# Performance work log

Hardware: AMD Instinct MI355X
Metric: run time of the kernel (lower is better)

Reference implementation:

```python
import jax, jax.numpy as jnp
import numpy as np

B, L, H, HD, FD = 1, 1024, 32, 64, 64
HID = H * HD
EPS = 1e-12


def setup_inputs() -> dict:
    key = jax.random.key(0)
    ks = jax.random.split(key, 7)
    s = 1.0 / np.sqrt(HID)
    return {
        "hidden_states": jax.random.normal(ks[0], (B, L, HID), dtype=jnp.float32),
        "Wq": jax.random.normal(ks[1], (HID, HID), dtype=jnp.float32) * s,
        "Wk": jax.random.normal(ks[2], (HID, HID), dtype=jnp.float32) * s,
        "Wv": jax.random.normal(ks[3], (HID, HID), dtype=jnp.float32) * s,
        "Wo": jax.random.normal(ks[4], (HID, HID), dtype=jnp.float32) * s,
        "Wfq": jax.random.normal(ks[5], (H, HD, FD), dtype=jnp.float32) * (1.0 / np.sqrt(HD)),
        "Wfk": jax.random.normal(ks[6], (H, HD, FD), dtype=jnp.float32) * (1.0 / np.sqrt(HD)),
    }


def _heads(x):
    # [b, l, hid] -> [b, h, l, hd]
    b, l, _ = x.shape
    return x.reshape(b, l, H, HD).transpose(0, 2, 1, 3)


def _feature_map(x, Wf):
    # per-head learned kernel + softmax over feature dim (hedgehog-style)
    z = jnp.einsum('bhld,hdf->bhlf', x, Wf)
    return jax.nn.softmax(z, axis=-1)


def _linear_attention(q, k, v, eps=EPS):
    # causal_dot_product: cumsum of outer-product KV state (fp32)
    qf, kf, vf = q.astype(jnp.float32), k.astype(jnp.float32), v.astype(jnp.float32)
    kv = jnp.cumsum(jnp.einsum('bhlf,bhld->bhlfd', kf, vf), axis=2)  # [b,h,l,f,d]
    y = jnp.einsum('bhlf,bhlfd->bhld', qf, kv)
    # fp32_attention=False branch: normalizer computed on cumsum(k)
    k_cum = jnp.cumsum(kf, axis=2).astype(q.dtype)
    denom = jnp.einsum('bhld,bhld->bhl', q, k_cum) + eps
    return y.astype(q.dtype) / denom[..., None]


def reference(hidden_states, Wq, Wk, Wv, Wo, Wfq, Wfk):
    b, l, _ = hidden_states.shape
    q = _heads(hidden_states @ Wq.T)
    k = _heads(hidden_states @ Wk.T)
    v = _heads(hidden_states @ Wv.T)
    fq = _feature_map(q, Wfq)
    fk = _feature_map(k, Wfk)
    y = _linear_attention(fq, fk, v)  # [b,h,l,hd]
    y = y.transpose(0, 2, 1, 3).reshape(b, l, HID)
    return y @ Wo.T
```

## Files before the change

kernel.cpp:

```cpp
#include <hip/hip_runtime.h>
#include <math.h>

constexpr int LQ  = 1024;
constexpr int NH  = 32;
constexpr int HDM = 64;
constexpr int FDM = 64;
constexpr int HID = 2048;
constexpr int NCH = 16;
constexpr int CT  = 64;
#define EPSV 1e-12f

typedef __bf16 bf16x8 __attribute__((ext_vector_type(8)));
typedef float  f32x4  __attribute__((ext_vector_type(4)));

__device__ __forceinline__ unsigned short f2b_raw(float x) {
    union { float f; unsigned int u; } v; v.f = x;
    unsigned int r = v.u + 0x7fffu + ((v.u >> 16) & 1u);
    return (unsigned short)(r >> 16);
}
__device__ __forceinline__ float b2f(ushort u) {
    union { unsigned int i; float f; } v; v.i = ((unsigned int)u) << 16; return v.f;
}

#define ASYNC16(ldsp, gp) __builtin_amdgcn_global_load_lds( \
    (const __attribute__((address_space(1))) void*)(gp),    \
    (__attribute__((address_space(3))) void*)(ldsp), 16, 0, 0)

template <bool BF16OUT>
__device__ __forceinline__ void gemm_body(const ushort* __restrict__ A,
                                          const ushort* __restrict__ B,
                                          void* __restrict__ Cv,
                                          int M, int N, int K) {
    __shared__ __align__(16) ushort As[64 * 32];
    __shared__ __align__(16) ushort Bs[128 * 32];
    const int t    = threadIdx.x;
    const int wave = t >> 6, lane = t & 63;
    const int wr   = (wave >> 1) * 32;
    const int wc   = (wave & 1) * 64;
    const int bm   = blockIdx.y * 64, bn = blockIdx.x * 128;

    const int lrow = lane >> 2;
    const int lk   = (lane & 3) * 8;
    const ushort* ga  = A + (size_t)(bm + wave * 16 + lrow) * K + lk;
    const ushort* gb0 = B + (size_t)(bn + wave * 32 + lrow) * K + lk;
    const ushort* gb1 = gb0 + 16 * (size_t)K;
    ushort* la  = As + (wave * 16) * 32;
    ushort* lb0 = Bs + (wave * 32) * 32;
    ushort* lb1 = lb0 + 16 * 32;

    const int fr = lane & 15;
    const int fo = (lane >> 4) * 8;

    f32x4 acc[2][4] = {};

    for (int k0 = 0; k0 < K; k0 += 32) {
        __syncthreads();
        ASYNC16(la, ga); ASYNC16(lb0, gb0); ASYNC16(lb1, gb1);
        ga += 32; gb0 += 32; gb1 += 32;
        __syncthreads();
        bf16x8 af[2], bg[4];
#pragma unroll
        for (int i = 0; i < 2; ++i) af[i] = *(const bf16x8*)&As[(wr + i * 16 + fr) * 32 + fo];
#pragma unroll
        for (int j = 0; j < 4; ++j) bg[j] = *(const bf16x8*)&Bs[(wc + j * 16 + fr) * 32 + fo];
#pragma unroll
        for (int i = 0; i < 2; ++i)
#pragma unroll
            for (int j = 0; j < 4; ++j)
                acc[i][j] = __builtin_amdgcn_mfma_f32_16x16x32_bf16(af[i], bg[j], acc[i][j], 0, 0, 0);
    }

    const int er = (lane >> 4) * 4;
    const int ec = lane & 15;
#pragma unroll
    for (int i = 0; i < 2; ++i)
#pragma unroll
        for (int j = 0; j < 4; ++j) {
            const size_t base = (size_t)(bm + wr + i * 16 + er) * N + bn + wc + j * 16 + ec;
            if constexpr (BF16OUT) {
                ushort* C = (ushort*)Cv;
#pragma unroll
                for (int r = 0; r < 4; ++r) C[base + (size_t)r * N] = f2b_raw(acc[i][j][r]);
            } else {
                float* C = (float*)Cv;
#pragma unroll
                for (int r = 0; r < 4; ++r) C[base + (size_t)r * N] = acc[i][j][r];
            }
        }
}

__global__ __launch_bounds__(256) void gemm_qkv(const ushort* __restrict__ hsb,
                                                const ushort* __restrict__ wqb,
                                                const ushort* __restrict__ wkb,
                                                const ushort* __restrict__ wvb,
                                                ushort* __restrict__ qb,
                                                ushort* __restrict__ kb,
                                                ushort* __restrict__ vb) {
    const ushort* B; ushort* C;
    if (blockIdx.z == 0)      { B = wqb; C = qb; }
    else if (blockIdx.z == 1) { B = wkb; C = kb; }
    else                      { B = wvb; C = vb; }
    gemm_body<true>(hsb, B, C, LQ, HID, HID);
}

__global__ __launch_bounds__(256) void gemm_one(const ushort* __restrict__ A,
                                                const ushort* __restrict__ B,
                                                float* __restrict__ C) {
    gemm_body<false>(A, B, C, LQ, HID, HID);
}

struct F2BArgs { const float* src[5]; ushort* dst[5]; int n[5]; };
__global__ __launch_bounds__(256) void f2b_multi(F2BArgs p) {
    const int which = blockIdx.y;
    const float* s = p.src[which];
    ushort* d = p.dst[which];
    const int n = p.n[which];
    const int i = (blockIdx.x * 256 + threadIdx.x) * 4;
    if (i >= n) return;
    float4 v = *(const float4*)&s[i];
    ushort4 o = make_ushort4(f2b_raw(v.x), f2b_raw(v.y), f2b_raw(v.z), f2b_raw(v.w));
    *(ushort4*)&d[i] = o;
}

__global__ __launch_bounds__(256) void wf_transpose(const float* __restrict__ Wfq,
                                                    const float* __restrict__ Wfk,
                                                    ushort* __restrict__ WfqT,
                                                    ushort* __restrict__ WfkT) {
    const int h = blockIdx.x, isK = blockIdx.y;
    const float* src = (isK ? Wfk : Wfq) + (size_t)h * 4096;
    ushort* dst = (isK ? WfkT : WfqT) + (size_t)h * 4096;
    __shared__ float tile[64][65];
    const int t = threadIdx.x;
    for (int it = 0; it < 16; ++it) {
        int e = it * 256 + t; int d = e >> 6, f = e & 63;
        tile[d][f] = src[e];
    }
    __syncthreads();
    for (int it = 0; it < 16; ++it) {
        int e = it * 256 + t; int f = e >> 6, d = e & 63;
        dst[e] = f2b_raw(tile[d][f]);
    }
}

__global__ __launch_bounds__(256) void featmap_chunk(
    const ushort* __restrict__ qb, const ushort* __restrict__ kb,
    const ushort* __restrict__ vb,
    const ushort* __restrict__ WfqT, const ushort* __restrict__ WfkT,
    ushort* __restrict__ fqB, ushort* __restrict__ fkB,
    ushort* __restrict__ VTb, float* __restrict__ Sraw, float* __restrict__ Ks) {
    __shared__ __align__(16) ushort Xs[64 * 72];
    __shared__ __align__(16) ushort Ws[64 * 72];
    __shared__ float Zs[64][68];
    __shared__ __align__(16) ushort Fs[64 * 72];
    __shared__ __align__(16) ushort Vs[64 * 72];

    const int c = blockIdx.x, h = blockIdx.y, isK = blockIdx.z;
    const int t = threadIdx.x, lane = t & 63, wave = t >> 6;
    const int l0 = c * CT;
    const int fr = lane & 15, fo = (lane >> 4) * 8;
    const int g = lane >> 4, cc = lane & 15;

    const ushort* X  = (isK ? kb : qb);
    const ushort* WT = (isK ? WfkT : WfqT) + (size_t)h * 4096;

    for (int it = 0; it < 2; ++it) {
        int e = (it * 256 + t) * 8;
        int row = e >> 6, col = e & 63;
        *(uint4*)&Xs[row * 72 + col] = *(const uint4*)&X[(size_t)(l0 + row) * HID + h * HDM + col];
        *(uint4*)&Ws[row * 72 + col] = *(const uint4*)&WT[e];
        if (isK) {
            uint4 vv = *(const uint4*)&vb[(size_t)(l0 + row) * HID + h * HDM + col];
            const ushort* pv = (const ushort*)&vv;
#pragma unroll
            for (int i = 0; i < 8; ++i) Vs[(col + i) * 72 + row] = pv[i];
        }
    }
    __syncthreads();

    f32x4 accZ[4] = {};
#pragma unroll
    for (int kp = 0; kp < 2; ++kp) {
        bf16x8 a = *(const bf16x8*)&Xs[(wave * 16 + fr) * 72 + kp * 32 + fo];
#pragma unroll
        for (int j = 0; j < 4; ++j) {
            bf16x8 b = *(const bf16x8*)&Ws[(j * 16 + fr) * 72 + kp * 32 + fo];
            accZ[j] = __builtin_amdgcn_mfma_f32_16x16x32_bf16(a, b, accZ[j], 0, 0, 0);
        }
    }
#pragma unroll
    for (int j = 0; j < 4; ++j)
#pragma unroll
        for (int r = 0; r < 4; ++r)
            Zs[wave * 16 + g * 4 + r][j * 16 + cc] = accZ[j][r];
    __syncthreads();

    const int srow = t >> 2, spart = t & 3;
    float zv[16], m = -1e30f;
#pragma unroll
    for (int i = 0; i < 16; ++i) { zv[i] = Zs[srow][spart * 16 + i]; m = fmaxf(m, zv[i]); }
    m = fmaxf(m, __shfl_xor(m, 1)); m = fmaxf(m, __shfl_xor(m, 2));
    float s = 0.f;
#pragma unroll
    for (int i = 0; i < 16; ++i) { zv[i] = __expf(zv[i] - m); s += zv[i]; }
    s += __shfl_xor(s, 1); s += __shfl_xor(s, 2);
    const float inv = 1.0f / s;
    ushort ov[16];
#pragma unroll
    for (int i = 0; i < 16; ++i) ov[i] = f2b_raw(zv[i] * inv);
    ushort* outp = (isK ? fkB : fqB) + ((size_t)h * LQ + l0 + srow) * FDM + spart * 16;
    *(uint4*)&outp[0] = *(uint4*)&ov[0];
    *(uint4*)&outp[8] = *(uint4*)&ov[8];
    if (isK) {
#pragma unroll
        for (int i = 0; i < 16; ++i) Fs[(spart * 16 + i) * 72 + srow] = ov[i];
    }
    if (!isK) return;
    __syncthreads();

    if (t < 64) {
        float ks = 0.f;
#pragma unroll 8
        for (int l = 0; l < 64; ++l) ks += b2f(Fs[t * 72 + l]);
        Ks[((size_t)h * NCH + c) * FDM + t] = ks;
    }
    const size_t cb = ((size_t)h * NCH + c) * 4096;
    for (int it = 0; it < 2; ++it) {
        int e = (it * 256 + t) * 8;
        int row = e >> 6, col = e & 63;
        *(uint4*)&VTb[cb + e] = *(const uint4*)&Vs[row * 72 + col];
    }
    f32x4 accS[4] = {};
#pragma unroll
    for (int kp = 0; kp < 2; ++kp) {
        bf16x8 a = *(const bf16x8*)&Vs[(wave * 16 + fr) * 72 + kp * 32 + fo];
#pragma unroll
        for (int j = 0; j < 4; ++j) {
            bf16x8 b = *(const bf16x8*)&Fs[(j * 16 + fr) * 72 + kp * 32 + fo];
            accS[j] = __builtin_amdgcn_mfma_f32_16x16x32_bf16(a, b, accS[j], 0, 0, 0);
        }
    }
    float* sp = Sraw + cb;
#pragma unroll
    for (int j = 0; j < 4; ++j)
#pragma unroll
        for (int r = 0; r < 4; ++r)
            sp[(wave * 16 + g * 4 + r) * 64 + j * 16 + cc] = accS[j][r];
}

__global__ __launch_bounds__(256) void prefix2(const float* __restrict__ Sraw,
                                               ushort* __restrict__ SpreB,
                                               const float* __restrict__ Ks,
                                               float* __restrict__ Kpre) {
    const int h = blockIdx.x, eb = blockIdx.y, t = threadIdx.x;
    const int e0 = eb * 512 + t * 2;
    float r0 = 0.f, r1 = 0.f;
    const size_t hb = (size_t)h * NCH * 4096;
    for (int c2 = 0; c2 < NCH; ++c2) {
        const size_t base = hb + (size_t)c2 * 4096 + e0;
        float c0 = Sraw[base], c1 = Sraw[base + 1];
        ushort2 o = make_ushort2(f2b_raw(r0), f2b_raw(r1));
        *(ushort2*)&SpreB[base] = o;
        r0 += c0; r1 += c1;
    }
    if (eb == 0 && t < 64) {
        float rk = 0.f;
        for (int c2 = 0; c2 < NCH; ++c2) {
            const size_t kb2 = ((size_t)h * NCH + c2) * FDM + t;
            float cur = Ks[kb2];
            Kpre[kb2] = rk;
            rk += cur;
        }
    }
}

__global__ __launch_bounds__(256) void intra2(
    const ushort* __restrict__ fqB, const ushort* __restrict__ fkB,
    const ushort* __restrict__ VTb, const ushort* __restrict__ SpreB,
    const float* __restrict__ Kpre, ushort* __restrict__ Yb) {
    __shared__ __align__(16) ushort fqs[64 * 72];
    __shared__ __align__(16) ushort fks[64 * 72];
    __shared__ __align__(16) ushort VTs[64 * 72];
    __shared__ __align__(16) ushort Sps[64 * 72];
    __shared__ __align__(16) ushort Pms[64 * 72];
    __shared__ float den[64], kpr[64];

    const int c = blockIdx.x, h = blockIdx.y;
    const int t = threadIdx.x, lane = t & 63, wave = t >> 6;
    const int l0 = c * CT;
    const int fr = lane & 15, fo = (lane >> 4) * 8;
    const int g = lane >> 4, cc = lane & 15;

    const size_t qkbase = ((size_t)h * LQ + l0) * FDM;
    const size_t cbase  = ((size_t)h * NCH + c) * 4096;
    for (int it = 0; it < 2; ++it) {
        int e = (it * 256 + t) * 8;
        int row = e >> 6, col = e & 63;
        *(uint4*)&fqs[row * 72 + col] = *(const uint4*)&fqB[qkbase + e];
        *(uint4*)&fks[row * 72 + col] = *(const uint4*)&fkB[qkbase + e];
        *(uint4*)&VTs[row * 72 + col] = *(const uint4*)&VTb[cbase + e];
        *(uint4*)&Sps[row * 72 + col] = *(const uint4*)&SpreB[cbase + e];
    }
    if (t < 64) kpr[t] = Kpre[((size_t)h * NCH + c) * FDM + t];
    __syncthreads();

    f32x4 accP[4] = {};
#pragma unroll
    for (int kp = 0; kp < 2; ++kp) {
        bf16x8 a = *(const bf16x8*)&fqs[(wave * 16 + fr) * 72 + kp * 32 + fo];
#pragma unroll
        for (int j = 0; j < 4; ++j) {
            bf16x8 b = *(const bf16x8*)&fks[(j * 16 + fr) * 72 + kp * 32 + fo];
            accP[j] = __builtin_amdgcn_mfma_f32_16x16x32_bf16(a, b, accP[j], 0, 0, 0);
        }
    }
#pragma unroll
    for (int j = 0; j < 4; ++j)
#pragma unroll
        for (int r = 0; r < 4; ++r) {
            int l = wave * 16 + g * 4 + r, lp = j * 16 + cc;
            Pms[l * 72 + lp] = (lp <= l) ? f2b_raw(accP[j][r]) : (ushort)0;
        }
    __syncthreads();

    {
        const int srow = t >> 2, spart = t & 3;
        float s = 0.f;
#pragma unroll
        for (int i = 0; i < 16; ++i) s += b2f(Pms[srow * 72 + spart * 16 + i]);
#pragma unroll
        for (int i = 0; i < 16; ++i) s += b2f(fqs[srow * 72 + spart * 16 + i]) * kpr[spart * 16 + i];
        s += __shfl_xor(s, 1); s += __shfl_xor(s, 2);
        if (spart == 0) den[srow] = s + EPSV;
    }
    __syncthreads();

    f32x4 accY[4] = {};
#pragma unroll
    for (int kp = 0; kp < 2; ++kp) {
        bf16x8 a = *(const bf16x8*)&Pms[(wave * 16 + fr) * 72 + kp * 32 + fo];
#pragma unroll
        for (int j = 0; j < 4; ++j) {
            bf16x8 b = *(const bf16x8*)&VTs[(j * 16 + fr) * 72 + kp * 32 + fo];
            accY[j] = __builtin_amdgcn_mfma_f32_16x16x32_bf16(a, b, accY[j], 0, 0, 0);
        }
    }
#pragma unroll
    for (int kp = 0; kp < 2; ++kp) {
        bf16x8 a = *(const bf16x8*)&fqs[(wave * 16 + fr) * 72 + kp * 32 + fo];
#pragma unroll
        for (int j = 0; j < 4; ++j) {
            bf16x8 b = *(const bf16x8*)&Sps[(j * 16 + fr) * 72 + kp * 32 + fo];
            accY[j] = __builtin_amdgcn_mfma_f32_16x16x32_bf16(a, b, accY[j], 0, 0, 0);
        }
    }
#pragma unroll
    for (int r = 0; r < 4; ++r) {
        int l = wave * 16 + g * 4 + r;
        float inv = 1.0f / den[l];
        ushort* yo = Yb + (size_t)(l0 + l) * HID + h * HDM;
#pragma unroll
        for (int j = 0; j < 4; ++j)
            yo[j * 16 + cc] = f2b_raw(accY[j][r] * inv);
    }
}

extern "C" void kernel_launch(void* const* d_in, const int* in_sizes, int n_in,
                              void* d_out, int out_size, void* d_ws, size_t ws_size,
                              hipStream_t stream) {
    const float* hs  = (const float*)d_in[0];
    const float* Wq  = (const float*)d_in[1];
    const float* Wk  = (const float*)d_in[2];
    const float* Wv  = (const float*)d_in[3];
    const float* Wo  = (const float*)d_in[4];
    const float* Wfq = (const float*)d_in[5];
    const float* Wfk = (const float*)d_in[6];
    float* out = (float*)d_out;

    const size_t SZ = (size_t)LQ * HID;
    const size_t WZ = (size_t)HID * HID;

    char* w = (char*)d_ws;
    auto aus = [&](size_t n) { ushort* p = (ushort*)w; w += n * sizeof(ushort); return p; };
    auto afl = [&](size_t n) { float*  p = (float*)w;  w += n * sizeof(float);  return p; };

    ushort* hsb   = aus(SZ);
    ushort* wqb   = aus(WZ);
    ushort* wkb   = aus(WZ);
    ushort* wvb   = aus(WZ);
    ushort* wob   = aus(WZ);
    ushort* qb2   = aus(SZ);
    ushort* kb2   = aus(SZ);
    ushort* vb2   = aus(SZ);
    ushort* fqB   = aus(SZ);
    ushort* fkB   = aus(SZ);
    ushort* VTb   = aus(SZ);
    ushort* WfqT  = aus((size_t)NH * 4096);
    ushort* WfkT  = aus((size_t)NH * 4096);
    ushort* SpreB = aus(SZ);
    ushort* Yb    = aus(SZ);
    float*  Sraw  = afl(SZ);
    float*  Ks    = afl((size_t)NH * NCH * FDM);
    float*  Kpre  = afl((size_t)NH * NCH * FDM);

    F2BArgs fa;
    fa.src[0] = hs; fa.dst[0] = hsb; fa.n[0] = (int)SZ;
    fa.src[1] = Wq; fa.dst[1] = wqb; fa.n[1] = (int)WZ;
    fa.src[2] = Wk; fa.dst[2] = wkb; fa.n[2] = (int)WZ;
    fa.src[3] = Wv; fa.dst[3] = wvb; fa.n[3] = (int)WZ;
    fa.src[4] = Wo; fa.dst[4] = wob; fa.n[4] = (int)WZ;
    f2b_multi<<<dim3((unsigned)(WZ / 1024), 5), 256, 0, stream>>>(fa);

    wf_transpose<<<dim3(NH, 2), 256, 0, stream>>>(Wfq, Wfk, WfqT, WfkT);

    gemm_qkv<<<dim3(HID / 128, LQ / 64, 3), 256, 0, stream>>>(hsb, wqb, wkb, wvb, qb2, kb2, vb2);

    featmap_chunk<<<dim3(NCH, NH, 2), 256, 0, stream>>>(qb2, kb2, vb2, WfqT, WfkT,
                                                        fqB, fkB, VTb, Sraw, Ks);

    prefix2<<<dim3(NH, 8), 256, 0, stream>>>(Sraw, SpreB, Ks, Kpre);

    intra2<<<dim3(NCH, NH), 256, 0, stream>>>(fqB, fkB, VTb, SpreB, Kpre, Yb);

    gemm_one<<<dim3(HID / 128, LQ / 64), 256, 0, stream>>>(Yb, wob, out);
}
```

Baseline: 212.8 us.

## Double-buffer GEMM LDS tiles with K=64 steps and XOR swizzle

Replaces the GEMM body with a templated core that uses double-buffered LDS tiles and steps K by 64 instead of 32. The next tile's async global-to-LDS loads are issued before computing on the current tile, which roughly halves the barriers per K step. An XOR swizzle on the LDS layout is meant to avoid bank conflicts. The output GEMM switches to 64x64 tiles to launch more blocks, at the cost of doubled shared memory and lower per-block reuse.

```diff
diff --git a/kernel.cpp b/kernel.cpp
--- a/kernel.cpp
+++ b/kernel.cpp
@@ -26,56 +26,85 @@
     (const __attribute__((address_space(1))) void*)(gp),    \
     (__attribute__((address_space(3))) void*)(ldsp), 16, 0, 0)
 
-template <bool BF16OUT>
-__device__ __forceinline__ void gemm_body(const ushort* __restrict__ A,
+template <int TM, int TN, bool BF16OUT>
+__device__ __forceinline__ void gemm_core(const ushort* __restrict__ A,
                                           const ushort* __restrict__ B,
                                           void* __restrict__ Cv,
                                           int M, int N, int K) {
-    __shared__ __align__(16) ushort As[64 * 32];
-    __shared__ __align__(16) ushort Bs[128 * 32];
-    const int t    = threadIdx.x;
-    const int wave = t >> 6, lane = t & 63;
-    const int wr   = (wave >> 1) * 32;
-    const int wc   = (wave & 1) * 64;
-    const int bm   = blockIdx.y * 64, bn = blockIdx.x * 128;
-
-    const int lrow = lane >> 2;
-    const int lk   = (lane & 3) * 8;
-    const ushort* ga  = A + (size_t)(bm + wave * 16 + lrow) * K + lk;
-    const ushort* gb0 = B + (size_t)(bn + wave * 32 + lrow) * K + lk;
-    const ushort* gb1 = gb0 + 16 * (size_t)K;
-    ushort* la  = As + (wave * 16) * 32;
-    ushort* lb0 = Bs + (wave * 32) * 32;
-    ushort* lb1 = lb0 + 16 * 32;
-
-    const int fr = lane & 15;
-    const int fo = (lane >> 4) * 8;
-
-    f32x4 acc[2][4] = {};
-
-    for (int k0 = 0; k0 < K; k0 += 32) {
-        __syncthreads();
-        ASYNC16(la, ga); ASYNC16(lb0, gb0); ASYNC16(lb1, gb1);
-        ga += 32; gb0 += 32; gb1 += 32;
-        __syncthreads();
-        bf16x8 af[2], bg[4];
-#pragma unroll
-        for (int i = 0; i < 2; ++i) af[i] = *(const bf16x8*)&As[(wr + i * 16 + fr) * 32 + fo];
-#pragma unroll
-        for (int j = 0; j < 4; ++j) bg[j] = *(const bf16x8*)&Bs[(wc + j * 16 + fr) * 32 + fo];
-#pragma unroll
-        for (int i = 0; i < 2; ++i)
-#pragma unroll
-            for (int j = 0; j < 4; ++j)
-                acc[i][j] = __builtin_amdgcn_mfma_f32_16x16x32_bf16(af[i], bg[j], acc[i][j], 0, 0, 0);
-    }
-
-    const int er = (lane >> 4) * 4;
+    constexpr int FI = TM / 32, FJ = TN / 32;
+    constexpr int AI = TM / 32, BJ = TN / 32;
+    constexpr int ASZ = TM * 64, BSZ = TN * 64;
+    __shared__ __align__(16) ushort As[2 * ASZ];
+    __shared__ __align__(16) ushort Bs[2 * BSZ];
+
+    const int t = threadIdx.x, wave = t >> 6, lane = t & 63;
+    const int wr = (wave >> 1) * (TM / 2), wc = (wave & 1) * (TN / 2);
+    const int bm = blockIdx.y * TM, bn = blockIdx.x * TN;
+
+    const int grow = lane >> 3;
+    const int gsw  = ((lane & 7) ^ (grow & 7)) << 3;
+    const int arow0 = wave * (TM / 4), brow0 = wave * (TN / 4);
+    const ushort* gA = A + (size_t)(bm + arow0 + grow) * K + gsw;
+    const ushort* gB = B + (size_t)(bn + brow0 + grow) * K + gsw;
+
+    const int fr = lane & 15, q = lane >> 4;
+
+    f32x4 acc[FI][FJ] = {};
+    const int NIT = K >> 6;
+
+    {
+        ushort* ab = As + arow0 * 64;
+        ushort* bb = Bs + brow0 * 64;
+#pragma unroll
+        for (int i = 0; i < AI; ++i) ASYNC16(ab + i * 512, gA + (size_t)i * 8 * K);
+#pragma unroll
+        for (int j = 0; j < BJ; ++j) ASYNC16(bb + j * 512, gB + (size_t)j * 8 * K);
+    }
+    __syncthreads();
+
+    for (int it = 0; it < NIT; ++it) {
+        const int p = it & 1;
+        if (it + 1 < NIT) {
+            const int ko = (it + 1) << 6;
+            ushort* ab = As + (p ^ 1) * ASZ + arow0 * 64;
+            ushort* bb = Bs + (p ^ 1) * BSZ + brow0 * 64;
+#pragma unroll
+            for (int i = 0; i < AI; ++i) ASYNC16(ab + i * 512, gA + ko + (size_t)i * 8 * K);
+#pragma unroll
+            for (int j = 0; j < BJ; ++j) ASYNC16(bb + j * 512, gB + ko + (size_t)j * 8 * K);
+        }
+        const ushort* ap = As + p * ASZ;
+        const ushort* bp = Bs + p * BSZ;
+        bf16x8 af[2][FI], bg[2][FJ];
+#pragma unroll
+        for (int ks = 0; ks < 2; ++ks) {
+#pragma unroll
+            for (int i = 0; i < FI; ++i) {
+                const int row = wr + i * 16 + fr;
+                af[ks][i] = *(const bf16x8*)&ap[row * 64 + ((((q + ks * 4)) ^ (row & 7)) << 3)];
+            }
+#pragma unroll
+            for (int j = 0; j < FJ; ++j) {
+                const int row = wc + j * 16 + fr;
+                bg[ks][j] = *(const bf16x8*)&bp[row * 64 + ((((q + ks * 4)) ^ (row & 7)) << 3)];
+            }
+        }
+#pragma unroll
+        for (int ks = 0; ks < 2; ++ks)
+#pragma unroll
+            for (int i = 0; i < FI; ++i)
+#pragma unroll
+                for (int j = 0; j < FJ; ++j)
+                    acc[i][j] = __builtin_amdgcn_mfma_f32_16x16x32_bf16(af[ks][i], bg[ks][j], acc[i][j], 0, 0, 0);
+        if (it + 1 < NIT) __syncthreads();
+    }
+
+    const int er = q * 4;
     const int ec = lane & 15;
 #pragma unroll
-    for (int i = 0; i < 2; ++i)
-#pragma unroll
-        for (int j = 0; j < 4; ++j) {
+    for (int i = 0; i < FI; ++i)
+#pragma unroll
+        for (int j = 0; j < FJ; ++j) {
             const size_t base = (size_t)(bm + wr + i * 16 + er) * N + bn + wc + j * 16 + ec;
             if constexpr (BF16OUT) {
                 ushort* C = (ushort*)Cv;
@@ -100,13 +129,13 @@
     if (blockIdx.z == 0)      { B = wqb; C = qb; }
     else if (blockIdx.z == 1) { B = wkb; C = kb; }
     else                      { B = wvb; C = vb; }
-    gemm_body<true>(hsb, B, C, LQ, HID, HID);
+    gemm_core<64, 128, true>(hsb, B, C, LQ, HID, HID);
 }
 
 __global__ __launch_bounds__(256) void gemm_one(const ushort* __restrict__ A,
                                                 const ushort* __restrict__ B,
                                                 float* __restrict__ C) {
-    gemm_body<false>(A, B, C, LQ, HID, HID);
+    gemm_core<64, 64, false>(A, B, C, LQ, HID, HID);
 }
 
 struct F2BArgs { const float* src[5]; ushort* dst[5]; int n[5]; };
@@ -421,5 +450,5 @@
 
     intra2<<<dim3(NCH, NH), 256, 0, stream>>>(fqB, fkB, VTb, SpreB, Kpre, Yb);
 
-    gemm_one<<<dim3(HID / 128, LQ / 64), 256, 0, stream>>>(Yb, wob, out);
-}
+    gemm_one<<<dim3(HID / 64, LQ / 64), 256, 0, stream>>>(Yb, wob, out);
+}
```

After: 198.5 us. 6.7% less time.
